# Performance work log

Measured on AMD Instinct MI355X. Metric: run time of the kernel, lower is better.

Reference implementation:

```python
import jax, jax.numpy as jnp
import numpy as np

# Hierarchy: 3 levels with 50 / 500 / 5000 classes, branching factor 10.
PIQUETS = (0, 50, 550, 5550)  # cumulative offsets per level
NB_LEVELS = 3
BATCH = 4096


def _make_parent():
    """parent[j] = global index of the parent of global node j (0 for roots).
    Encodes the same structure as the dense H matrix (H[p, j] = 1 iff parent[j] == p)."""
    parent = np.zeros(PIQUETS[-1], dtype=np.int32)
    parent[PIQUETS[1]:PIQUETS[2]] = np.arange(500) // 10            # level-1 -> level-0
    parent[PIQUETS[2]:PIQUETS[3]] = PIQUETS[1] + np.arange(5000) // 10  # level-2 -> level-1
    return jnp.asarray(parent)


def setup_inputs() -> dict:
    key = jax.random.key(0)
    k1, k2 = jax.random.split(key)
    y_pred = jax.random.normal(k1, (BATCH, PIQUETS[-1]), dtype=jnp.float32)
    target = jax.random.randint(k2, (BATCH,), 0, 5000)  # local leaf-level indices
    return {"y_pred": y_pred, "target": target, "parent": _make_parent()}


def reference(y_pred, target, parent):
    # children_preds[b, p] = sum of child logits of node p
    # == (H[:piquets[-2], :] @ y_pred.T).T, exploiting H's one-parent sparsity.
    children = jax.ops.segment_sum(
        y_pred.T[PIQUETS[1]:], parent[PIQUETS[1]:], num_segments=PIQUETS[-2]
    ).T  # (B, piquets[-2])

    levels_pred = [y_pred[:, PIQUETS[k]:PIQUETS[k + 1]] for k in range(NB_LEVELS)]
    levels_children = [children[:, PIQUETS[k]:PIQUETS[k + 1]] for k in range(NB_LEVELS - 1)]
    log_p = [jax.nn.log_softmax(l, axis=1) for l in levels_pred]
    log_c = [jax.nn.log_softmax(l, axis=1) for l in levels_children]

    # Ancestor targets per level (vectorized replacement for get_grandparents loops)
    g = target.astype(jnp.int32) + PIQUETS[-2]  # global leaf index
    globs = [g]
    for _ in range(NB_LEVELS - 1):
        globs.append(parent[globs[-1]])
    globs = globs[::-1]  # level 0 .. level L-1, global indices
    loc = [globs[k] - PIQUETS[k] for k in range(NB_LEVELS)]  # local per-level targets

    def ce(logp, tgt):
        return -jnp.take_along_axis(logp, tgt[:, None], axis=1).mean()

    def kl_mean(logp, logq):
        # torch KLDivLoss(reduction='mean'): mean over ALL elements of q*(log q - log p)
        return jnp.mean(jnp.exp(logq) * (logq - logp))

    loss = jnp.float32(0.0)
    kl_penalty = jnp.float32(0.0)
    for k in range(NB_LEVELS - 1):
        kl_penalty += 0.5 * (kl_mean(log_p[k], log_c[k]) + kl_mean(log_c[k], log_p[k]))
        loss += 0.5 * ce(log_p[k], loc[k])
    loss += 0.5 * ce(log_p[-1], loc[-1])
    loss += 0.5 * kl_penalty
    return loss
```

## Files before the change

### kernel.cpp

```cpp
#include <hip/hip_runtime.h>

#define BATCH 4096
#define ROW   5550
#define WSPAN 1388

typedef const __attribute__((address_space(1))) void glb_void;
typedef __attribute__((address_space(3))) void lds_void;

__device__ __forceinline__ float wave_sum(float v) {
    #pragma unroll
    for (int off = 32; off; off >>= 1) v += __shfl_xor(v, off, 64);
    return v;
}

__global__ __launch_bounds__(256)
void hjsd_kernel(const float* __restrict__ y, const int* __restrict__ tgt,
                 float* __restrict__ P) {
    __shared__ __align__(16) float s_buf[5552];

    const int b    = blockIdx.x;
    const int tid  = threadIdx.x;
    const int w    = tid >> 6;
    const int lane = tid & 63;

    int t = 0;
    if (tid == 0) t = tgt[b];

    const int    ofs = (b & 1) ? 2 : 0;
    const float* gb  = y + (size_t)b * ROW - ofs;
    {
        const float* gw = gb + WSPAN * w;
        float*       lw = s_buf + WSPAN * w;
        #pragma unroll
        for (int c = 0; c < 5; ++c)
            __builtin_amdgcn_global_load_lds((glb_void*)(gw + 256 * c + 4 * lane),
                                             (lds_void*)(lw + 256 * c), 16, 0, 0);
        if (lane < 27)
            __builtin_amdgcn_global_load_lds((glb_void*)(gw + 1280 + 4 * lane),
                                             (lds_void*)(lw + 1280), 16, 0, 0);
    }
    asm volatile("s_waitcnt vmcnt(0)" ::: "memory");
    __syncthreads();

    const float* s_row = s_buf + ofs;
    const float* s1    = s_row + 50;
    const float* s2    = s_row + 550;

    float E2=0.f, EC1=0.f, E1=0.f, EC0=0.f, E0=0.f;
    float S11=0.f, S21=0.f, S10=0.f, S20=0.f, Y=0.f;

    if (tid < 250) {
        const float2* g0 = reinterpret_cast<const float2*>(s2 + 20 * tid);
        const float2* g1 = g0 + 5;
        const int r = tid % 5;
        float c0 = 0.f, c1 = 0.f;
        #pragma unroll
        for (int j = 0; j < 5; ++j) {
            int s = r + j; if (s >= 5) s -= 5;
            float2 a = g0[s], d = g1[s];
            c0 += a.x + a.y;
            c1 += d.x + d.y;
            E2 += __expf(a.x) + __expf(a.y) + __expf(d.x) + __expf(d.y);
        }
        float ec0 = __expf(c0), ec1 = __expf(c1);
        EC1 = ec0 + ec1;
        float2 xab = *reinterpret_cast<const float2*>(s1 + 2 * tid);
        float ea = __expf(xab.x), eb = __expf(xab.y);
        E1  = ea + eb;
        S11 = ec0 * (c0 - xab.x) + ec1 * (c1 - xab.y);
        S21 = ea * (xab.x - c0) + eb * (xab.y - c1);
    }

    if (tid < 50) {
        const float2* p1 = reinterpret_cast<const float2*>(s1 + 10 * tid);
        const int r = tid % 5;
        float c = 0.f;
        #pragma unroll
        for (int j = 0; j < 5; ++j) {
            int s = r + j; if (s >= 5) s -= 5;
            float2 a = p1[s];
            c += a.x + a.y;
        }
        float ec = __expf(c);
        float x0 = s_row[tid];
        float e0 = __expf(x0);
        EC0 = ec; E0 = e0;
        S10 = ec * (c - x0);
        S20 = e0 * (x0 - c);
    }

    if (tid == 0) Y = s2[t] + s1[t / 10] + s_row[t / 100];

    float sums[9] = {E2, EC1, E1, EC0, E0, S11, S21, S10, S20};
    #pragma unroll
    for (int k = 0; k < 9; ++k) sums[k] = wave_sum(sums[k]);

    if (lane == 0) {
        float* dst = P + (size_t)b * 48 + 12 * w;
        *reinterpret_cast<float4*>(dst)     = make_float4(sums[0], sums[1], sums[2], sums[3]);
        *reinterpret_cast<float4*>(dst + 4) = make_float4(sums[4], sums[5], sums[6], sums[7]);
        *reinterpret_cast<float2*>(dst + 8) = make_float2(sums[8], Y);
    }
}

__global__ __launch_bounds__(256)
void reduce1(const float* __restrict__ P, float* __restrict__ part) {
    __shared__ float scr[4];
    const int tid = threadIdx.x;
    const int b   = blockIdx.x * 256 + tid;
    const float4* q4 = reinterpret_cast<const float4*>(P + (size_t)b * 48);
    float t9[10];
    #pragma unroll
    for (int k = 0; k < 10; ++k) t9[k] = 0.f;
    #pragma unroll
    for (int w = 0; w < 4; ++w) {
        float4 A = q4[3 * w], B = q4[3 * w + 1], C = q4[3 * w + 2];
        t9[0] += A.x; t9[1] += A.y; t9[2] += A.z; t9[3] += A.w;
        t9[4] += B.x; t9[5] += B.y; t9[6] += B.z; t9[7] += B.w;
        t9[8] += C.x; t9[9] += C.y;
    }
    float loss = 0.5f * (__logf(t9[0]) + __logf(t9[2]) + __logf(t9[4]) - t9[9])
               + (0.25f / 500.0f) * (t9[5] / t9[1] + t9[6] / t9[2])
               + (0.25f / 50.0f)  * (t9[7] / t9[3] + t9[8] / t9[4]);
    loss = wave_sum(loss);
    if ((tid & 63) == 0) scr[tid >> 6] = loss;
    __syncthreads();
    if (tid == 0) part[blockIdx.x] = scr[0] + scr[1] + scr[2] + scr[3];
}

__global__ __launch_bounds__(64)
void reduce2(const float* __restrict__ part, float* __restrict__ out) {
    float s = (threadIdx.x < 16) ? part[threadIdx.x] : 0.f;
    s = wave_sum(s);
    if (threadIdx.x == 0) out[0] = s * (1.0f / BATCH);
}

extern "C" void kernel_launch(void* const* d_in, const int* in_sizes, int n_in,
                              void* d_out, int out_size, void* d_ws, size_t ws_size,
                              hipStream_t stream) {
    const float* y   = (const float*)d_in[0];
    const int*   tgt = (const int*)d_in[1];
    float* out  = (float*)d_out;
    float* P    = (float*)d_ws;
    float* part = (float*)d_ws + (size_t)BATCH * 48;

    hjsd_kernel<<<BATCH, 256, 0, stream>>>(y, tgt, P);
    reduce1<<<16, 256, 0, stream>>>(P, part);
    reduce2<<<1, 64, 0, stream>>>(part, out);
}
```

Baseline: 139.2 us.

## Rebalance leaf-group work across waves and start before the block barrier

Measured after the change: 140.0 us. About the same (+0.5%).

```diff
diff --git a/kernel.cpp b/kernel.cpp
--- a/kernel.cpp
+++ b/kernel.cpp
@@ -24,7 +24,7 @@
     const int lane = tid & 63;
 
     int t = 0;
-    if (tid == 0) t = tgt[b];
+    if (tid == 53) t = tgt[b];
 
     const int    ofs = (b & 1) ? 2 : 0;
     const float* gb  = y + (size_t)b * ROW - ofs;
@@ -40,66 +40,93 @@
                                              (lds_void*)(lw + 1280), 16, 0, 0);
     }
     asm volatile("s_waitcnt vmcnt(0)" ::: "memory");
-    __syncthreads();
+    __builtin_amdgcn_sched_barrier(0);
 
     const float* s_row = s_buf + ofs;
-    const float* s1    = s_row + 50;
-    const float* s2    = s_row + 550;
 
     float E2=0.f, EC1=0.f, E1=0.f, EC0=0.f, E0=0.f;
     float S11=0.f, S21=0.f, S10=0.f, S20=0.f, Y=0.f;
 
-    if (tid < 250) {
-        const float2* g0 = reinterpret_cast<const float2*>(s2 + 20 * tid);
-        const float2* g1 = g0 + 5;
-        const int r = tid % 5;
-        float c0 = 0.f, c1 = 0.f;
-        #pragma unroll
-        for (int j = 0; j < 5; ++j) {
-            int s = r + j; if (s >= 5) s -= 5;
-            float2 a = g0[s], d = g1[s];
-            c0 += a.x + a.y;
-            c1 += d.x + d.y;
-            E2 += __expf(a.x) + __expf(a.y) + __expf(d.x) + __expf(d.y);
-        }
-        float ec0 = __expf(c0), ec1 = __expf(c1);
-        EC1 = ec0 + ec1;
-        float2 xab = *reinterpret_cast<const float2*>(s1 + 2 * tid);
-        float ea = __expf(xab.x), eb = __expf(xab.y);
-        E1  = ea + eb;
-        S11 = ec0 * (c0 - xab.x) + ec1 * (c1 - xab.y);
-        S21 = ea * (xab.x - c0) + eb * (xab.y - c1);
-    }
-
-    if (tid < 50) {
-        const float2* p1 = reinterpret_cast<const float2*>(s1 + 10 * tid);
-        const int r = tid % 5;
+    auto group_sum = [&](int g, float& cout) {
+        const float2* p = reinterpret_cast<const float2*>(s_row + 550 + 10 * g);
+        const int r = lane % 5;
         float c = 0.f;
         #pragma unroll
         for (int j = 0; j < 5; ++j) {
             int s = r + j; if (s >= 5) s -= 5;
-            float2 a = p1[s];
-            c += a.x + a.y;
+            float2 a = p[s];
+            c  += a.x + a.y;
+            E2 += __expf(a.x) + __expf(a.y);
         }
-        float ec = __expf(c);
-        float x0 = s_row[tid];
-        float e0 = __expf(x0);
-        EC0 = ec; E0 = e0;
-        S10 = ec * (c - x0);
-        S20 = e0 * (x0 - c);
+        cout = c;
+    };
+
+    const int  gbase = (w == 0) ? 0 : 84 + 139 * (w - 1);
+    const int  gA = gbase + lane;
+    const int  gB = gbase + 64 + lane;
+    const int  gC = gbase + 128 + lane;
+    const bool hasB = (w == 0) ? (lane < 19) : true;
+    const bool hasC = (w != 0) && (lane < 10);
+    float cA = 0.f, cB = 0.f, cC = 0.f;
+    group_sum(gA, cA);
+    if (hasB) group_sum(gB, cB);
+    if (hasC) group_sum(gC, cC);
+
+    __syncthreads();
+
+    auto pair_term = [&](int g, float c) {
+        float x  = s_row[50 + g];
+        float ec = __expf(c), ex = __expf(x);
+        EC1 += ec; E1 += ex;
+        S11 += ec * (c - x);
+        S21 += ex * (x - c);
+    };
+    pair_term(gA, cA);
+    if (hasB) pair_term(gB, cB);
+    if (hasC) pair_term(gC, cC);
+
+    if (w == 0) {
+        if (lane < 50) {
+            const float2* p1 = reinterpret_cast<const float2*>(s_row + 50 + 10 * lane);
+            const int r = lane % 5;
+            float c = 0.f;
+            #pragma unroll
+            for (int j = 0; j < 5; ++j) {
+                int s = r + j; if (s >= 5) s -= 5;
+                float2 a = p1[s];
+                c += a.x + a.y;
+            }
+            float ec = __expf(c);
+            float x0 = s_row[lane];
+            float e0 = __expf(x0);
+            EC0 = ec; E0 = e0;
+            S10 = ec * (c - x0);
+            S20 = e0 * (x0 - c);
+        } else if (lane < 53) {
+            int g = 83 + 139 * (lane - 50);
+            const float2* p = reinterpret_cast<const float2*>(s_row + 550 + 10 * g);
+            float c = 0.f;
+            #pragma unroll
+            for (int j = 0; j < 5; ++j) {
+                float2 a = p[j];
+                c  += a.x + a.y;
+                E2 += __expf(a.x) + __expf(a.y);
+            }
+            pair_term(g, c);
+        } else if (lane == 53) {
+            Y = s_row[550 + t] + s_row[50 + t / 10] + s_row[t / 100];
+        }
     }
 
-    if (tid == 0) Y = s2[t] + s1[t / 10] + s_row[t / 100];
-
-    float sums[9] = {E2, EC1, E1, EC0, E0, S11, S21, S10, S20};
+    float sums[10] = {E2, EC1, E1, EC0, E0, S11, S21, S10, S20, Y};
     #pragma unroll
-    for (int k = 0; k < 9; ++k) sums[k] = wave_sum(sums[k]);
+    for (int k = 0; k < 10; ++k) sums[k] = wave_sum(sums[k]);
 
     if (lane == 0) {
         float* dst = P + (size_t)b * 48 + 12 * w;
         *reinterpret_cast<float4*>(dst)     = make_float4(sums[0], sums[1], sums[2], sums[3]);
         *reinterpret_cast<float4*>(dst + 4) = make_float4(sums[4], sums[5], sums[6], sums[7]);
-        *reinterpret_cast<float2*>(dst + 8) = make_float2(sums[8], Y);
+        *reinterpret_cast<float2*>(dst + 8) = make_float2(sums[8], sums[9]);
     }
 }
 
```
